# Kernel tuning notes

Hardware: AMD Instinct MI355X
Metric: run time of the kernel (lower is better)

The kernel has to match this reference:

```python
import jax, jax.numpy as jnp
import numpy as np

B = 16384          # batch
N_IN = 1024        # input nodes
L = 8              # layers
W_LAYER = 512      # nodes per layer (fan-in and fan-out)
N_NODES = N_IN + L * W_LAYER  # 5120 total nodes in shared buffer
MASK_DENSITY = 0.25


def setup_inputs() -> dict:
    key = jax.random.key(0)
    kx, kw, km, kb = jax.random.split(key, 4)
    x = jax.random.normal(kx, (B, N_IN), dtype=jnp.float32)
    W = jax.random.normal(kw, (L, W_LAYER, W_LAYER), dtype=jnp.float32) * 0.05
    mask = (jax.random.uniform(km, (L, W_LAYER, W_LAYER)) < MASK_DENSITY).astype(jnp.float32)
    bias = jax.random.normal(kb, (L, W_LAYER), dtype=jnp.float32) * 0.01
    rng = np.random.default_rng(0)
    # layer l gathers from nodes already computed: indices in [0, N_IN + l*W_LAYER)
    in_idx = np.stack([rng.integers(0, N_IN + l * W_LAYER, size=W_LAYER) for l in range(L)]).astype(np.int32)
    # layer l writes its own contiguous node slots
    out_idx = np.stack([np.arange(N_IN + l * W_LAYER, N_IN + (l + 1) * W_LAYER) for l in range(L)]).astype(np.int32)
    return {"x": x, "W": W, "mask": mask, "bias": bias,
            "in_idx": jnp.asarray(in_idx), "out_idx": jnp.asarray(out_idx)}


def reference(x, W, mask, bias, in_idx, out_idx):
    # shared node-value buffer, inputs written into first N_IN columns
    values = jnp.zeros((x.shape[0], N_NODES), dtype=x.dtype)
    values = values.at[:, :N_IN].set(x)

    def step(vals, layer):
        idx_in, idx_out, Wl, ml, bl = layer
        node_inputs = vals[:, idx_in]                       # [B, W_LAYER] gather
        h = jax.nn.relu(node_inputs @ (Wl * ml).T + bl)     # masked linear + ReLU
        return vals.at[:, idx_out].set(h), None             # scatter back

    values, _ = jax.lax.scan(step, values, (in_idx, out_idx, W, mask, bias))
    return values[:, out_idx[-1]]  # output nodes = last layer's nodes
```

## Files before the change

kernel.cpp:

```cpp
#include <hip/hip_runtime.h>
#include <stdint.h>

typedef unsigned short u16;
typedef unsigned int   u32;
typedef short s16x8 __attribute__((ext_vector_type(8)));
typedef float f32x4 __attribute__((ext_vector_type(4)));

#define NB    16384
#define NIN   1024
#define WLY   512
#define NLAY  8
#define NNODE (NIN + NLAY * WLY)
#define BN    64

__device__ __forceinline__ u16 f2bf(float f) {
  union { float f; u32 u; } c; c.f = f;
  return (u16)((c.u + 0x7fffu + ((c.u >> 16) & 1u)) >> 16);
}
__device__ __forceinline__ float bf2f(u16 h) {
  union { u32 u; float f; } c; c.u = ((u32)h) << 16;
  return c.f;
}

#define SCHED0() __builtin_amdgcn_sched_barrier(0)
#define BAR()    __builtin_amdgcn_s_barrier()
#define WAITLG0() asm volatile("s_waitcnt lgkmcnt(0)" ::: "memory")

__global__ void prep_w(const float* __restrict__ W, const float* __restrict__ Mk,
                       u16* __restrict__ Wm) {
  int id   = blockIdx.x * 256 + threadIdx.x;
  int lane = id & 63;
  int chunk = id >> 6;
  int kf = chunk & 1;
  int mb = (chunk >> 1) & 31;
  int kt = (chunk >> 6) & 7;
  int l  = chunk >> 9;
  int m  = (mb << 4) + (lane & 15);
  int k0 = (kt << 6) + (kf << 5) + ((lane >> 4) << 3);
  size_t base = ((size_t)l << 18) + (size_t)m * 512 + k0;
  const float4* w4 = (const float4*)(W + base);
  const float4* k4 = (const float4*)(Mk + base);
  float4 w0 = w4[0], w1 = w4[1];
  float4 k0v = k4[0], k1v = k4[1];
  u32 p0 = (u32)f2bf(w0.x * k0v.x) | ((u32)f2bf(w0.y * k0v.y) << 16);
  u32 p1 = (u32)f2bf(w0.z * k0v.z) | ((u32)f2bf(w0.w * k0v.w) << 16);
  u32 p2 = (u32)f2bf(w1.x * k1v.x) | ((u32)f2bf(w1.y * k1v.y) << 16);
  u32 p3 = (u32)f2bf(w1.z * k1v.z) | ((u32)f2bf(w1.w * k1v.w) << 16);
  uint4 v; v.x = p0; v.y = p1; v.z = p2; v.w = p3;
  *(uint4*)(Wm + ((size_t)chunk << 9) + (lane << 3)) = v;
}

__global__ __launch_bounds__(512, 2) void fused_net(
    const float* __restrict__ x, const u16* __restrict__ Wfrag,
    const float* __restrict__ bias, const int* __restrict__ in_idx,
    u16* __restrict__ V, float* __restrict__ out) {

  __shared__ __align__(16) u16 Graw[2][64 * 72];
  __shared__ __align__(16) u16 Gswz[2][4096];
  __shared__ __align__(16) u16 Ebuf[512 * 72];

  int t = threadIdx.x;
  int lane = t & 63, w = t >> 6;
  int mlane = lane & 15, g = lane >> 4;
  int n0 = blockIdx.x * BN;
  int krow  = (w << 3) + (lane >> 3);
  int kcol8 = lane & 7;

  float* xt = (float*)Ebuf;
  for (int cc = 0; cc < 8; ++cc) {
    #pragma unroll
    for (int it = 0; it < 4; ++it) {
      int cl = t + it * 512;
      int b = cl >> 5, p = cl & 31;
      *(float4*)(xt + b * 128 + (p << 2)) =
          *(const float4*)(x + (size_t)(n0 + b) * 1024 + cc * 128 + (p << 2));
    }
    __syncthreads();
    {
      int c = t >> 2, seg = t & 3;
      u32 p[8];
      #pragma unroll
      for (int i = 0; i < 8; ++i) {
        u16 lo = f2bf(xt[(seg * 16 + 2 * i) * 128 + c]);
        u16 hi = f2bf(xt[(seg * 16 + 2 * i + 1) * 128 + c]);
        p[i] = (u32)lo | ((u32)hi << 16);
      }
      u16* dst = V + (size_t)(cc * 128 + c) * NB + n0 + seg * 16;
      uint4 v0; v0.x = p[0]; v0.y = p[1]; v0.z = p[2]; v0.w = p[3];
      uint4 v1; v1.x = p[4]; v1.y = p[5]; v1.z = p[6]; v1.w = p[7];
      *(uint4*)dst = v0;
      *(uint4*)(dst + 8) = v1;
    }
    __syncthreads();
  }

#define GLD(KT) (*(const uint4*)(V + (size_t)rowv[KT] * NB + n0 + (kcol8 << 3)))

#define STW(KT) do {                                                           \
    *(uint4*)((char*)Graw[(KT) & 1] + krow * 144 + (kcol8 << 4)) =             \
        gv[(KT) & 1];                                                          \
  } while (0)

#define TRANSP(KT) do {                                                        \
    const u16* gb_ = Graw[(KT) & 1];                                           \
    u32 p0_ = (u32)gb_[(w * 8 + 0) * 72 + lane] |                              \
              ((u32)gb_[(w * 8 + 1) * 72 + lane] << 16);                       \
    u32 p1_ = (u32)gb_[(w * 8 + 2) * 72 + lane] |                              \
              ((u32)gb_[(w * 8 + 3) * 72 + lane] << 16);                       \
    u32 p2_ = (u32)gb_[(w * 8 + 4) * 72 + lane] |                              \
              ((u32)gb_[(w * 8 + 5) * 72 + lane] << 16);                       \
    u32 p3_ = (u32)gb_[(w * 8 + 6) * 72 + lane] |                              \
              ((u32)gb_[(w * 8 + 7) * 72 + lane] << 16);                       \
    uint4 vv_; vv_.x = p0_; vv_.y = p1_; vv_.z = p2_; vv_.w = p3_;             \
    *(uint4*)((char*)Gswz[(KT) & 1] + lane * 128 +                             \
              ((w * 16) ^ ((lane & 7) << 4))) = vv_;                           \
  } while (0)

#define LDA(KTN) do {                                                          \
    _Pragma("unroll") for (int mb = 0; mb < 4; ++mb)                           \
    _Pragma("unroll") for (int kf = 0; kf < 2; ++kf)                           \
      a[(KTN) & 1][mb][kf] = *(const s16x8*)(Wl +                              \
          ((size_t)((((KTN) * 32 + (w << 2) + mb) << 1) + kf) << 9) +          \
          (lane << 3));                                                        \
  } while (0)

#define MM(KT) do {                                                            \
    const char* gs_ = (const char*)Gswz[(KT) & 1];                             \
    _Pragma("unroll") for (int kf = 0; kf < 2; ++kf) {                         \
      s16x8 bfr[4];                                                            \
      _Pragma("unroll") for (int nf = 0; nf < 4; ++nf) {                       \
        int n_ = (nf << 4) + mlane;                                            \
        bfr[nf] = *(const s16x8*)(gs_ + n_ * 128 +                             \
                  (((kf << 6) + (g << 4)) ^ ((n_ & 7) << 4)));                 \
      }                                                                        \
      _Pragma("unroll") for (int mb = 0; mb < 4; ++mb)                         \
      _Pragma("unroll") for (int nf = 0; nf < 4; ++nf)                         \
        acc[mb][nf] = __builtin_amdgcn_mfma_f32_16x16x32_bf16(                 \
            a[(KT) & 1][mb][kf], bfr[nf], acc[mb][nf], 0, 0, 0);               \
    }                                                                          \
  } while (0)

  for (int l = 0; l < NLAY; ++l) {
    __syncthreads();

    int rowv[8];
    #pragma unroll
    for (int kt = 0; kt < 8; ++kt)
      rowv[kt] = in_idx[(l << 9) + (kt << 6) + krow];

    const u16* Wl = Wfrag + ((size_t)l << 18);
    int node_out = NIN + l * WLY;

    f32x4 acc[4][4];
    #pragma unroll
    for (int i = 0; i < 4; ++i)
      #pragma unroll
      for (int j = 0; j < 4; ++j)
        acc[i][j] = (f32x4){0.f, 0.f, 0.f, 0.f};

    s16x8 a[2][4][2];
    uint4 gv[2];

    gv[0] = GLD(0);
    LDA(0);
    STW(0);
    TRANSP(0);
    gv[1] = GLD(1);
    SCHED0(); WAITLG0(); BAR(); SCHED0();

    #pragma unroll
    for (int kt = 0; kt < 8; ++kt) {
      if (kt + 2 < 8) gv[kt & 1] = GLD(kt + 2);
      if (kt + 1 < 8) LDA(kt + 1);
      MM(kt);
      if (kt + 1 < 8) {
        STW(kt + 1);
        TRANSP(kt + 1);
      }
      SCHED0(); WAITLG0(); BAR(); SCHED0();
    }

    if (l < NLAY - 1) {
      #pragma unroll
      for (int mb = 0; mb < 4; ++mb) {
        float4 bv = *(const float4*)(bias + (l << 9) + (w << 6) + (mb << 4) + (g << 2));
        float bvr[4] = {bv.x, bv.y, bv.z, bv.w};
        #pragma unroll
        for (int nf = 0; nf < 4; ++nf)
          #pragma unroll
          for (int r = 0; r < 4; ++r) {
            int m = (w << 6) + (mb << 4) + (g << 2) + r;
            int n = (nf << 4) + mlane;
            Ebuf[m * 72 + n] = f2bf(fmaxf(acc[mb][nf][r] + bvr[r], 0.f));
          }
      }
      #pragma unroll
      for (int it = 0; it < 8; ++it) {
        int row = (w << 6) + (it << 3) + (lane >> 3);
        uint4 vv = *(uint4*)(Ebuf + row * 72 + ((lane & 7) << 3));
        *(uint4*)(V + (size_t)(node_out + row) * NB + n0 + ((lane & 7) << 3)) = vv;
      }
    } else {
      #pragma unroll
      for (int mb = 0; mb < 4; ++mb) {
        float4 bv = *(const float4*)(bias + (l << 9) + (w << 6) + (mb << 4) + (g << 2));
        float bvr[4] = {bv.x, bv.y, bv.z, bv.w};
        #pragma unroll
        for (int nf = 0; nf < 4; ++nf)
          #pragma unroll
          for (int r = 0; r < 4; ++r) {
            int m = (w << 6) + (mb << 4) + (g << 2) + r;
            int n = (nf << 4) + mlane;
            Ebuf[m * 66 + n] = f2bf(fmaxf(acc[mb][nf][r] + bvr[r], 0.f));
          }
      }
      __syncthreads();
      #pragma unroll
      for (int pn = 0; pn < 8; ++pn)
        #pragma unroll
        for (int h = 0; h < 2; ++h) {
          int n = (t >> 6) + (pn << 3);
          int mbase = ((t & 63) << 2) + (h << 8);
          float4 v;
          v.x = bf2f(Ebuf[(mbase + 0) * 66 + n]);
          v.y = bf2f(Ebuf[(mbase + 1) * 66 + n]);
          v.z = bf2f(Ebuf[(mbase + 2) * 66 + n]);
          v.w = bf2f(Ebuf[(mbase + 3) * 66 + n]);
          *(float4*)(out + (size_t)(n0 + n) * 512 + mbase) = v;
        }
    }
  }
#undef GLD
#undef STW
#undef TRANSP
#undef LDA
#undef MM
}

extern "C" void kernel_launch(void* const* d_in, const int* in_sizes, int n_in,
                              void* d_out, int out_size, void* d_ws, size_t ws_size,
                              hipStream_t stream) {
  (void)in_sizes; (void)n_in; (void)out_size; (void)ws_size;
  const float* x    = (const float*)d_in[0];
  const float* W    = (const float*)d_in[1];
  const float* Mk   = (const float*)d_in[2];
  const float* bias = (const float*)d_in[3];
  const int*  inidx = (const int*)d_in[4];
  float* out = (float*)d_out;

  char* ws = (char*)d_ws;
  u16* V     = (u16*)ws;
  u16* Wfrag = (u16*)(ws + (size_t)NNODE * NB * 2);

  prep_w<<<dim3(1024), 256, 0, stream>>>(W, Mk, Wfrag);
  fused_net<<<dim3(256), 512, 0, stream>>>(x, Wfrag, bias, inidx, V, out);
}
```

Measured before the change: 114.2 us.

## Stage whole layer gather in LDS up front, drop per-k-tile barriers

Replaces the double-buffered per-k-tile gather/transpose pipeline with a single upfront phase. All 8 gathered tiles are loaded, written and transposed into one large shared pool, followed by a single barrier, so the MFMA loop runs without any barriers. The next layer's in_idx rows are prefetched during the current layer. LDS use grows to about 136 KB per block, which likely lowers occupancy to one block per CU. It also removes the overlap between global gather loads and MFMA work.

```diff
diff --git a/kernel.cpp b/kernel.cpp
--- a/kernel.cpp
+++ b/kernel.cpp
@@ -22,7 +22,6 @@
   return c.f;
 }
 
-#define SCHED0() __builtin_amdgcn_sched_barrier(0)
 #define BAR()    __builtin_amdgcn_s_barrier()
 #define WAITLG0() asm volatile("s_waitcnt lgkmcnt(0)" ::: "memory")
 
@@ -55,9 +54,9 @@
     const float* __restrict__ bias, const int* __restrict__ in_idx,
     u16* __restrict__ V, float* __restrict__ out) {
 
-  __shared__ __align__(16) u16 Graw[2][64 * 72];
-  __shared__ __align__(16) u16 Gswz[2][4096];
-  __shared__ __align__(16) u16 Ebuf[512 * 72];
+  __shared__ __align__(16) char pool[139264];
+  u16* Graw = (u16*)pool;
+  u16* Gswz = (u16*)(pool + 73728);
 
   int t = threadIdx.x;
   int lane = t & 63, w = t >> 6;
@@ -66,7 +65,7 @@
   int krow  = (w << 3) + (lane >> 3);
   int kcol8 = lane & 7;
 
-  float* xt = (float*)Ebuf;
+  float* xt = (float*)pool;
   for (int cc = 0; cc < 8; ++cc) {
     #pragma unroll
     for (int it = 0; it < 4; ++it) {
@@ -94,15 +93,8 @@
     __syncthreads();
   }
 
-#define GLD(KT) (*(const uint4*)(V + (size_t)rowv[KT] * NB + n0 + (kcol8 << 3)))
-
-#define STW(KT) do {                                                           \
-    *(uint4*)((char*)Graw[(KT) & 1] + krow * 144 + (kcol8 << 4)) =             \
-        gv[(KT) & 1];                                                          \
-  } while (0)
-
 #define TRANSP(KT) do {                                                        \
-    const u16* gb_ = Graw[(KT) & 1];                                           \
+    const u16* gb_ = Graw + (KT) * 4608;                                       \
     u32 p0_ = (u32)gb_[(w * 8 + 0) * 72 + lane] |                              \
               ((u32)gb_[(w * 8 + 1) * 72 + lane] << 16);                       \
     u32 p1_ = (u32)gb_[(w * 8 + 2) * 72 + lane] |                              \
@@ -112,7 +104,7 @@
     u32 p3_ = (u32)gb_[(w * 8 + 6) * 72 + lane] |                              \
               ((u32)gb_[(w * 8 + 7) * 72 + lane] << 16);                       \
     uint4 vv_; vv_.x = p0_; vv_.y = p1_; vv_.z = p2_; vv_.w = p3_;             \
-    *(uint4*)((char*)Gswz[(KT) & 1] + lane * 128 +                             \
+    *(uint4*)((char*)Gswz + lane * 1024 + ((KT) << 7) +                        \
               ((w * 16) ^ ((lane & 7) << 4))) = vv_;                           \
   } while (0)
 
@@ -125,12 +117,12 @@
   } while (0)
 
 #define MM(KT) do {                                                            \
-    const char* gs_ = (const char*)Gswz[(KT) & 1];                             \
+    const char* gs_ = (const char*)Gswz + ((KT) << 7);                         \
     _Pragma("unroll") for (int kf = 0; kf < 2; ++kf) {                         \
       s16x8 bfr[4];                                                            \
       _Pragma("unroll") for (int nf = 0; nf < 4; ++nf) {                       \
         int n_ = (nf << 4) + mlane;                                            \
-        bfr[nf] = *(const s16x8*)(gs_ + n_ * 128 +                             \
+        bfr[nf] = *(const s16x8*)(gs_ + n_ * 1024 +                            \
                   (((kf << 6) + (g << 4)) ^ ((n_ & 7) << 4)));                 \
       }                                                                        \
       _Pragma("unroll") for (int mb = 0; mb < 4; ++mb)                         \
@@ -140,17 +132,42 @@
     }                                                                          \
   } while (0)
 
+  int rowv[8];
+  #pragma unroll
+  for (int kt = 0; kt < 8; ++kt)
+    rowv[kt] = in_idx[(kt << 6) + krow];
+
   for (int l = 0; l < NLAY; ++l) {
     __syncthreads();
 
-    int rowv[8];
-    #pragma unroll
-    for (int kt = 0; kt < 8; ++kt)
-      rowv[kt] = in_idx[(l << 9) + (kt << 6) + krow];
-
     const u16* Wl = Wfrag + ((size_t)l << 18);
     int node_out = NIN + l * WLY;
 
+    s16x8 a[2][4][2];
+
+    uint4 gv[8];
+    #pragma unroll
+    for (int kt = 0; kt < 8; ++kt)
+      gv[kt] = *(const uint4*)(V + (size_t)rowv[kt] * NB + n0 + (kcol8 << 3));
+    LDA(0);
+    #pragma unroll
+    for (int kt = 0; kt < 8; ++kt)
+      *(uint4*)((char*)Graw + kt * 9216 + krow * 144 + (kcol8 << 4)) = gv[kt];
+    #pragma unroll
+    for (int kt = 0; kt < 8; ++kt) { TRANSP(kt); }
+
+    WAITLG0(); BAR();
+
+    int rowvn[8];
+    if (l + 1 < NLAY) {
+      #pragma unroll
+      for (int kt = 0; kt < 8; ++kt)
+        rowvn[kt] = in_idx[((l + 1) << 9) + (kt << 6) + krow];
+    } else {
+      #pragma unroll
+      for (int kt = 0; kt < 8; ++kt) rowvn[kt] = 0;
+    }
+
     f32x4 acc[4][4];
     #pragma unroll
     for (int i = 0; i < 4; ++i)
@@ -158,28 +175,16 @@
       for (int j = 0; j < 4; ++j)
         acc[i][j] = (f32x4){0.f, 0.f, 0.f, 0.f};
 
-    s16x8 a[2][4][2];
-    uint4 gv[2];
-
-    gv[0] = GLD(0);
-    LDA(0);
-    STW(0);
-    TRANSP(0);
-    gv[1] = GLD(1);
-    SCHED0(); WAITLG0(); BAR(); SCHED0();
-
     #pragma unroll
     for (int kt = 0; kt < 8; ++kt) {
-      if (kt + 2 < 8) gv[kt & 1] = GLD(kt + 2);
-      if (kt + 1 < 8) LDA(kt + 1);
+      if (kt < 7) LDA(kt + 1);
       MM(kt);
-      if (kt + 1 < 8) {
-        STW(kt + 1);
-        TRANSP(kt + 1);
-      }
-      SCHED0(); WAITLG0(); BAR(); SCHED0();
-    }
-
+    }
+
+    #pragma unroll
+    for (int kt = 0; kt < 8; ++kt) rowv[kt] = rowvn[kt];
+
+    u16* Ebuf = (u16*)pool;
     if (l < NLAY - 1) {
       #pragma unroll
       for (int mb = 0; mb < 4; ++mb) {
@@ -230,8 +235,6 @@
         }
     }
   }
-#undef GLD
-#undef STW
 #undef TRANSP
 #undef LDA
 #undef MM
```

Result: slower. 143.9 us (+26.0%).

## Process two K-tiles per barrier stage with four-deep operand buffers

Applied to the files above, without the earlier changes.

The per-layer K loop now handles two 64-wide K-tiles between barriers instead of one. This halves the number of workgroup barriers and wait-for-loads points per layer. To support it, the swizzled LDS tiles, gathered-row registers and weight-fragment registers are now four-deep instead of two-deep. The trade-off is more VGPR pressure (roughly twice the weight-fragment registers, with possible spills under the launch bound) and more LDS per block, in exchange for longer stretches of MFMA work with fewer synchronisations.

```diff
diff --git a/kernel.cpp b/kernel.cpp
--- a/kernel.cpp
+++ b/kernel.cpp
@@ -56,7 +56,7 @@
     u16* __restrict__ V, float* __restrict__ out) {
 
   __shared__ __align__(16) u16 Graw[2][64 * 72];
-  __shared__ __align__(16) u16 Gswz[2][4096];
+  __shared__ __align__(16) u16 Gswz[4][4096];
   __shared__ __align__(16) u16 Ebuf[512 * 72];
 
   int t = threadIdx.x;
@@ -94,11 +94,14 @@
     __syncthreads();
   }
 
-#define GLD(KT) (*(const uint4*)(V + (size_t)rowv[KT] * NB + n0 + (kcol8 << 3)))
+#define GLD(KT) do {                                                           \
+    gv[(KT) & 3] =                                                             \
+        *(const uint4*)(V + (size_t)rowv[KT] * NB + n0 + (kcol8 << 3));        \
+  } while (0)
 
 #define STW(KT) do {                                                           \
     *(uint4*)((char*)Graw[(KT) & 1] + krow * 144 + (kcol8 << 4)) =             \
-        gv[(KT) & 1];                                                          \
+        gv[(KT) & 3];                                                          \
   } while (0)
 
 #define TRANSP(KT) do {                                                        \
@@ -112,20 +115,20 @@
     u32 p3_ = (u32)gb_[(w * 8 + 6) * 72 + lane] |                              \
               ((u32)gb_[(w * 8 + 7) * 72 + lane] << 16);                       \
     uint4 vv_; vv_.x = p0_; vv_.y = p1_; vv_.z = p2_; vv_.w = p3_;             \
-    *(uint4*)((char*)Gswz[(KT) & 1] + lane * 128 +                             \
+    *(uint4*)((char*)Gswz[(KT) & 3] + lane * 128 +                             \
               ((w * 16) ^ ((lane & 7) << 4))) = vv_;                           \
   } while (0)
 
 #define LDA(KTN) do {                                                          \
     _Pragma("unroll") for (int mb = 0; mb < 4; ++mb)                           \
     _Pragma("unroll") for (int kf = 0; kf < 2; ++kf)                           \
-      a[(KTN) & 1][mb][kf] = *(const s16x8*)(Wl +                              \
+      a[(KTN) & 3][mb][kf] = *(const s16x8*)(Wl +                              \
           ((size_t)((((KTN) * 32 + (w << 2) + mb) << 1) + kf) << 9) +          \
           (lane << 3));                                                        \
   } while (0)
 
 #define MM(KT) do {                                                            \
-    const char* gs_ = (const char*)Gswz[(KT) & 1];                             \
+    const char* gs_ = (const char*)Gswz[(KT) & 3];                             \
     _Pragma("unroll") for (int kf = 0; kf < 2; ++kf) {                         \
       s16x8 bfr[4];                                                            \
       _Pragma("unroll") for (int nf = 0; nf < 4; ++nf) {                       \
@@ -136,7 +139,7 @@
       _Pragma("unroll") for (int mb = 0; mb < 4; ++mb)                         \
       _Pragma("unroll") for (int nf = 0; nf < 4; ++nf)                         \
         acc[mb][nf] = __builtin_amdgcn_mfma_f32_16x16x32_bf16(                 \
-            a[(KT) & 1][mb][kf], bfr[nf], acc[mb][nf], 0, 0, 0);               \
+            a[(KT) & 3][mb][kf], bfr[nf], acc[mb][nf], 0, 0, 0);               \
     }                                                                          \
   } while (0)
 
@@ -158,27 +161,37 @@
       for (int j = 0; j < 4; ++j)
         acc[i][j] = (f32x4){0.f, 0.f, 0.f, 0.f};
 
-    s16x8 a[2][4][2];
-    uint4 gv[2];
-
-    gv[0] = GLD(0);
-    LDA(0);
-    STW(0);
-    TRANSP(0);
-    gv[1] = GLD(1);
-    SCHED0(); WAITLG0(); BAR(); SCHED0();
-
-    #pragma unroll
-    for (int kt = 0; kt < 8; ++kt) {
-      if (kt + 2 < 8) gv[kt & 1] = GLD(kt + 2);
-      if (kt + 1 < 8) LDA(kt + 1);
-      MM(kt);
-      if (kt + 1 < 8) {
-        STW(kt + 1);
-        TRANSP(kt + 1);
-      }
-      SCHED0(); WAITLG0(); BAR(); SCHED0();
-    }
+    s16x8 a[4][4][2];
+    uint4 gv[4];
+
+    GLD(0); GLD(1);
+    LDA(0); LDA(1);
+    STW(0); STW(1);
+    TRANSP(0); TRANSP(1);
+    GLD(2); GLD(3);
+    SCHED0(); WAITLG0(); BAR(); SCHED0();
+
+    GLD(4); GLD(5);
+    LDA(2); LDA(3);
+    MM(0); MM(1);
+    STW(2); STW(3);
+    TRANSP(2); TRANSP(3);
+    SCHED0(); WAITLG0(); BAR(); SCHED0();
+
+    GLD(6); GLD(7);
+    LDA(4); LDA(5);
+    MM(2); MM(3);
+    STW(4); STW(5);
+    TRANSP(4); TRANSP(5);
+    SCHED0(); WAITLG0(); BAR(); SCHED0();
+
+    LDA(6); LDA(7);
+    MM(4); MM(5);
+    STW(6); STW(7);
+    TRANSP(6); TRANSP(7);
+    SCHED0(); WAITLG0(); BAR(); SCHED0();
+
+    MM(6); MM(7);
 
     if (l < NLAY - 1) {
       #pragma unroll
```

New measurement: 108.8 us, median of 2. -4.7%, faster.
